# Kernel optimization log

Measured on AMD Instinct MI355X. Metric: run time of the kernel, lower is better.

The kernel has to match this reference:

```python
import jax, jax.numpy as jnp
import numpy as np

N = 4096      # num_nodes (single graph; batch is all-zeros in the original when absent)
CIN = 1024    # in_channels
H = 1024      # hidden_channels
COUT = 512    # out_channels
R = 10        # nodevec rank (hardcoded in the module)
BN_EPS = 1e-5


def setup_inputs() -> dict:
    key = jax.random.key(0)
    ks = jax.random.split(key, 8)
    w = lambda k, shp: jax.random.normal(k, shp, dtype=jnp.float32) * 0.02
    return {
        "x": jax.random.normal(ks[0], (N, CIN), dtype=jnp.float32),
        "w_map": w(ks[1], (CIN, H)),
        "b_map": jnp.zeros((H,), jnp.float32),
        "nv1": jax.random.normal(ks[2], (N, R), dtype=jnp.float32),
        "nv2": jax.random.normal(ks[3], (R, N), dtype=jnp.float32),
        "w1": w(ks[4], (H, H)),
        "b1": jnp.zeros((H,), jnp.float32),
        "w2": w(ks[5], (H, COUT)),
        "b2": jnp.zeros((COUT,), jnp.float32),
        "bn1_g": jnp.ones((H,), jnp.float32),
        "bn1_b": jnp.zeros((H,), jnp.float32),
        "bn1_m": jnp.zeros((H,), jnp.float32),
        "bn1_v": jnp.ones((H,), jnp.float32),
        "bn2_g": jnp.ones((COUT,), jnp.float32),
        "bn2_b": jnp.zeros((COUT,), jnp.float32),
        "bn2_m": jnp.zeros((COUT,), jnp.float32),
        "bn2_v": jnp.ones((COUT,), jnp.float32),
        "w_attn": w(ks[6], (COUT, 1)),
        "b_attn": jnp.zeros((1,), jnp.float32),
    }


def _batchnorm_eval(h, g, b, m, v):
    # BatchNorm1d in eval mode: running stats
    return (h - m) * jax.lax.rsqrt(v + BN_EPS) * g + b


def reference(x, w_map, b_map, nv1, nv2, w1, b1, w2, b2,
              bn1_g, bn1_b, bn1_m, bn1_v, bn2_g, bn2_b, bn2_m, bn2_v,
              w_attn, b_attn):
    # feature mapping
    xm = jax.nn.relu(x @ w_map + b_map)                       # [N, H]
    # adaptive adjacency: softmax(relu(nv1 @ nv2), dim=1) -> strictly positive,
    # so nonzero() yields the fully dense edge list; we keep it dense.
    adp = jax.nn.softmax(jax.nn.relu(nv1 @ nv2), axis=1)      # [N, N]
    # gcn_norm (PyG GCNConv default): add unit self-loops, normalize by
    # column-degree^-1/2 on both sides.
    A = adp + jnp.eye(N, dtype=adp.dtype)                      # [N, N]
    deg = jnp.sum(A, axis=0)                                   # column sums (target degree)
    dinv = jnp.where(deg > 0, jax.lax.rsqrt(deg), 0.0)
    An = (dinv[:, None] * A) * dinv[None, :]                   # D^-1/2 A D^-1/2
    # GCNConv: out_i = sum_j An[j, i] * (x W)_j + bias  =>  An^T @ (X W) + b
    h = jax.nn.relu(An.T @ (xm @ w1) + b1)                     # conv1 + relu
    h = _batchnorm_eval(h, bn1_g, bn1_b, bn1_m, bn1_v)         # bn1 (dropout off in eval)
    h = jax.nn.relu(An.T @ (h @ w2) + b2)                      # conv2 + relu
    h = _batchnorm_eval(h, bn2_g, bn2_b, bn2_m, bn2_v)         # bn2
    # global_mean_pool with batch == zeros -> single-graph mean
    pooled = jnp.mean(h, axis=0, keepdims=True)                # [1, COUT]
    attn = jax.nn.sigmoid(pooled @ w_attn + b_attn)            # [1, 1]
    return pooled * attn                                       # [1, COUT]
```

## Files before the change

kernel.cpp:

```cpp
#include <hip/hip_runtime.h>

#define NN 4096
#define R_RANK 10

typedef __bf16 bf16x8 __attribute__((ext_vector_type(8)));
typedef float floatx4 __attribute__((ext_vector_type(4)));

__device__ __forceinline__ unsigned short f2bf(float f) {
    union { float f; unsigned int u; } v; v.f = f;
    unsigned int r = v.u + 0x7FFFu + ((v.u >> 16) & 1u);
    return (unsigned short)(r >> 16);
}
__device__ __forceinline__ void gll16(const void* g, void* l) {
    __builtin_amdgcn_global_load_lds(
        (const __attribute__((address_space(1))) unsigned int*)g,
        (__attribute__((address_space(3))) unsigned int*)l, 16, 0, 0);
}
template<int N>
__device__ __forceinline__ void wait_vm() {
    if constexpr (N == 0)       asm volatile("s_waitcnt vmcnt(0)" ::: "memory");
    else if constexpr (N == 3)  asm volatile("s_waitcnt vmcnt(3)" ::: "memory");
    else if constexpr (N == 4)  asm volatile("s_waitcnt vmcnt(4)" ::: "memory");
    else if constexpr (N == 6)  asm volatile("s_waitcnt vmcnt(6)" ::: "memory");
    else if constexpr (N == 8)  asm volatile("s_waitcnt vmcnt(8)" ::: "memory");
    else static_assert(N < 0, "add vmcnt literal");
}
#define SB __builtin_amdgcn_sched_barrier(0)

__global__ __launch_bounds__(256) void row_stats_kernel(
    const float* __restrict__ nv1, const float* __restrict__ nv2,
    float* __restrict__ rowmax, float* __restrict__ rowsum,
    float* __restrict__ deg, float* __restrict__ pooled)
{
    const int i0 = blockIdx.x * 4;
    const int tid = threadIdx.x;
    if (blockIdx.x < 16) deg[blockIdx.x * 256 + tid] = 0.f;
    if (blockIdx.x >= 16 && blockIdx.x < 18) pooled[(blockIdx.x - 16) * 256 + tid] = 0.f;
    __shared__ float a[4][R_RANK];
    if (tid < 4 * R_RANK) a[tid / R_RANK][tid % R_RANK] = nv1[i0 * R_RANK + tid];
    __syncthreads();

    float s[4][16];
    float mx[4] = {0.f, 0.f, 0.f, 0.f};
    #pragma unroll
    for (int t = 0; t < 16; ++t) {
        const int j = t * 256 + tid;
        float v[R_RANK];
        #pragma unroll
        for (int r = 0; r < R_RANK; ++r) v[r] = nv2[r * NN + j];
        #pragma unroll
        for (int q = 0; q < 4; ++q) {
            float acc = 0.f;
            #pragma unroll
            for (int r = 0; r < R_RANK; ++r) acc = fmaf(a[q][r], v[r], acc);
            acc = fmaxf(acc, 0.f);
            s[q][t] = acc;
            mx[q] = fmaxf(mx[q], acc);
        }
    }
    __shared__ float red[4][4];
    #pragma unroll
    for (int q = 0; q < 4; ++q) {
        float m = mx[q];
        #pragma unroll
        for (int off = 32; off > 0; off >>= 1) m = fmaxf(m, __shfl_down(m, off, 64));
        if ((tid & 63) == 0) red[q][tid >> 6] = m;
    }
    __syncthreads();
    #pragma unroll
    for (int q = 0; q < 4; ++q)
        mx[q] = fmaxf(fmaxf(red[q][0], red[q][1]), fmaxf(red[q][2], red[q][3]));
    __syncthreads();
    float sm[4] = {0.f, 0.f, 0.f, 0.f};
    #pragma unroll
    for (int t = 0; t < 16; ++t)
        #pragma unroll
        for (int q = 0; q < 4; ++q) sm[q] += __expf(s[q][t] - mx[q]);
    #pragma unroll
    for (int q = 0; q < 4; ++q) {
        float m = sm[q];
        #pragma unroll
        for (int off = 32; off > 0; off >>= 1) m += __shfl_down(m, off, 64);
        if ((tid & 63) == 0) red[q][tid >> 6] = m;
    }
    __syncthreads();
    if (tid < 4) {
        rowmax[i0 + tid] = mx[tid];
        rowsum[i0 + tid] = red[tid][0] + red[tid][1] + red[tid][2] + red[tid][3];
    }
}

__global__ __launch_bounds__(256) void col_sum_kernel(
    const float* __restrict__ nv1, const float* __restrict__ nv2,
    const float* __restrict__ rowmax, const float* __restrict__ rowsum,
    float* __restrict__ deg)
{
    const int tid = threadIdx.x;
    const int j = blockIdx.x * 256 + tid;
    const int i0 = blockIdx.y * 64;
    __shared__ float a[64][R_RANK];
    __shared__ float rm[64], rs[64];
    if (tid < 64) {
        rm[tid] = rowmax[i0 + tid];
        rs[tid] = 1.0f / rowsum[i0 + tid];
    }
    for (int t = tid; t < 64 * R_RANK; t += 256)
        a[t / R_RANK][t % R_RANK] = nv1[i0 * R_RANK + t];
    __syncthreads();

    float v[R_RANK];
    #pragma unroll
    for (int r = 0; r < R_RANK; ++r) v[r] = nv2[r * NN + j];
    float acc = 0.f;
    #pragma unroll 4
    for (int t = 0; t < 64; ++t) {
        float s = 0.f;
        #pragma unroll
        for (int r = 0; r < R_RANK; ++r) s = fmaf(a[t][r], v[r], s);
        s = fmaxf(s, 0.f);
        acc += __expf(s - rm[t]) * rs[t];
    }
    atomicAdd(&deg[j], acc);
}

__global__ __launch_bounds__(256) void an_build_kernel(
    const float* __restrict__ nv1, const float* __restrict__ nv2,
    const float* __restrict__ rowmax, const float* __restrict__ rowsum,
    const float* __restrict__ deg, unsigned short* __restrict__ AnT)
{
    const int tid = threadIdx.x;
    const int j = blockIdx.x * 256 + tid;
    const int i0 = blockIdx.y * 8;
    __shared__ float v2s[8][R_RANK];
    __shared__ float dis[8];
    if (tid < 8 * R_RANK) {
        const int r = tid / 8, t = tid % 8;
        v2s[t][r] = nv2[r * NN + i0 + t];
    }
    if (tid < 8) dis[tid] = rsqrtf(1.0f + deg[i0 + tid]);

    float a[R_RANK];
    #pragma unroll
    for (int r = 0; r < R_RANK; ++r) a[r] = nv1[j * R_RANK + r];
    const float rm = rowmax[j];
    const float rs = 1.0f / rowsum[j];
    const float dj = rsqrtf(1.0f + deg[j]);
    __syncthreads();

    #pragma unroll
    for (int t = 0; t < 8; ++t) {
        const int i = i0 + t;
        float s = 0.f;
        #pragma unroll
        for (int r = 0; r < R_RANK; ++r) s = fmaf(a[r], v2s[t][r], s);
        s = fmaxf(s, 0.f);
        const float adp = __expf(s - rm) * rs;
        const float val = (adp + ((i == j) ? 1.f : 0.f)) * dis[t] * dj;
        AnT[(size_t)i * NN + j] = f2bf(val);
    }
}

__global__ __launch_bounds__(256) void prep_kernel(
    const float* __restrict__ x, const float* __restrict__ w_map,
    const float* __restrict__ w1, const float* __restrict__ w2,
    unsigned short* __restrict__ xb, unsigned short* __restrict__ wmT,
    unsigned short* __restrict__ w1T, unsigned short* __restrict__ w2T)
{
    const int z = blockIdx.z;
    const int tid = threadIdx.x;
    if (z == 3) {
        const int b = blockIdx.x + blockIdx.y * 32;
        const size_t base = (size_t)b * 4096 + (size_t)tid * 16;
        #pragma unroll
        for (int i = 0; i < 2; ++i) {
            const float4 a0 = *(const float4*)(x + base + i * 8);
            const float4 a1 = *(const float4*)(x + base + i * 8 + 4);
            ushort4 p, q;
            p.x = f2bf(a0.x); p.y = f2bf(a0.y); p.z = f2bf(a0.z); p.w = f2bf(a0.w);
            q.x = f2bf(a1.x); q.y = f2bf(a1.y); q.z = f2bf(a1.z); q.w = f2bf(a1.w);
            *(ushort4*)(xb + base + i * 8) = p;
            *(ushort4*)(xb + base + i * 8 + 4) = q;
        }
        return;
    }
    const float* W = (z == 0) ? w_map : (z == 1) ? w1 : w2;
    unsigned short* WT = (z == 0) ? wmT : (z == 1) ? w1T : w2T;
    const int CN = (z == 2) ? 512 : 1024;
    if (blockIdx.x * 32 >= CN) return;
    __shared__ float s[32][33];
    const int tx = tid & 31, ty = tid >> 5;
    const int r0 = blockIdx.y * 32, c0 = blockIdx.x * 32;
    #pragma unroll
    for (int i = 0; i < 4; ++i)
        s[ty + 8 * i][tx] = W[(size_t)(r0 + ty + 8 * i) * CN + c0 + tx];
    __syncthreads();
    #pragma unroll
    for (int i = 0; i < 4; ++i)
        WT[(size_t)(c0 + ty + 8 * i) * 1024 + r0 + tx] = f2bf(s[tx][ty + 8 * i]);
}

template<int OUTM, int EPI, int SK>
__global__ __launch_bounds__(512) void gemm_mfma(
    const unsigned short* __restrict__ A, const unsigned short* __restrict__ Bt,
    void* __restrict__ Out, const int M, const int N, const int K,
    const float* __restrict__ bias, const float* __restrict__ gamma,
    const float* __restrict__ beta, const float* __restrict__ mean,
    const float* __restrict__ var)
{
    __shared__ __align__(16) unsigned short As[2][8192];
    __shared__ __align__(16) unsigned short Bs[2][8192];
    const int tid = threadIdx.x;
    const int l = tid & 63, w = tid >> 6;
    const int wy = w >> 2, wx = w & 3;
    const int lr = l & 15, lq = l >> 4;

    const int gx = gridDim.x, gy = gridDim.y;
    int lin = blockIdx.x + gx * (blockIdx.y + gy * blockIdx.z);
    const int q = (gx * gy * gridDim.z) >> 3;
    lin = (lin & 7) * q + (lin >> 3);
    const int bx = lin % gx;
    const int by = (lin / gx) % gy;
    const int bz = lin / (gx * gy);

    const int row0 = by * 128, col0 = bx * 128;
    const int Kc = K / SK;
    const int kb = bz * Kc;
    const int nt = Kc >> 6;

    const unsigned short* Ag0 = A + (size_t)(row0 + w * 16 + lr) * K + kb + lq * 8;
    const unsigned short* Bg0 = Bt + (size_t)(col0 + w * 16 + lr) * K + kb + lq * 8;

    floatx4 acc[4][2];
    #pragma unroll
    for (int i = 0; i < 4; ++i)
        #pragma unroll
        for (int j = 0; j < 2; ++j) acc[i][j] = (floatx4){0.f, 0.f, 0.f, 0.f};

    #define STAGE(b, t)                                                         \
    {                                                                           \
        char* Aw = (char*)As[b] + w * 1024;                                     \
        char* Bw = (char*)Bs[b] + w * 1024;                                     \
        const int kk = (t) * 64;                                                \
        gll16(Ag0 + kk,      Aw);                                               \
        gll16(Ag0 + kk + 32, Aw + 8192);                                        \
        gll16(Bg0 + kk,      Bw);                                               \
        gll16(Bg0 + kk + 32, Bw + 8192);                                        \
    }

    STAGE(0, 0)
    for (int t = 0; t < nt; ++t) {
        if (t + 1 < nt) {
            STAGE((t + 1) & 1, t + 1)
            wait_vm<4>();
        } else {
            wait_vm<0>();
        }
        SB; __builtin_amdgcn_s_barrier(); SB;

        const char* Afr = (const char*)As[t & 1] + wy * 4096 + l * 16;
        const char* Bfr = (const char*)Bs[t & 1] + wx * 2048 + l * 16;
        #pragma unroll
        for (int h = 0; h < 2; ++h) {
            bf16x8 af[4], bf[2];
            #pragma unroll
            for (int i = 0; i < 4; ++i) af[i] = *(const bf16x8*)(Afr + h * 8192 + i * 1024);
            #pragma unroll
            for (int j = 0; j < 2; ++j) bf[j] = *(const bf16x8*)(Bfr + h * 8192 + j * 1024);
            #pragma unroll
            for (int mf = 0; mf < 4; ++mf)
                #pragma unroll
                for (int nf = 0; nf < 2; ++nf)
                    acc[mf][nf] = __builtin_amdgcn_mfma_f32_16x16x32_bf16(
                        af[mf], bf[nf], acc[mf][nf], 0, 0, 0);
        }
        SB; __builtin_amdgcn_s_barrier(); SB;
    }
    #undef STAGE

    const int gr0 = row0 + wy * 64 + lq * 4;
    const int gc0 = col0 + wx * 32 + lr;
    if constexpr (OUTM == 0) {
        float* Pz = (float*)Out + (size_t)bz * M * N;
        #pragma unroll
        for (int mf = 0; mf < 4; ++mf) {
            const int gr = gr0 + mf * 16;
            #pragma unroll
            for (int nf = 0; nf < 2; ++nf) {
                const int gc = gc0 + nf * 16;
                #pragma unroll
                for (int r = 0; r < 4; ++r)
                    Pz[(size_t)(gr + r) * N + gc] = acc[mf][nf][r];
            }
        }
    } else {
        unsigned short* O = (unsigned short*)Out;
        #pragma unroll
        for (int nf = 0; nf < 2; ++nf) {
            const int gc = gc0 + nf * 16;
            float bb = 0.f, sc = 1.f, sh = 0.f;
            if constexpr (EPI >= 1) bb = bias[gc];
            if constexpr (EPI == 2) {
                sc = gamma[gc] * rsqrtf(var[gc] + 1e-5f);
                sh = beta[gc] - mean[gc] * sc;
            }
            #pragma unroll
            for (int mf = 0; mf < 4; ++mf) {
                const int gr = gr0 + mf * 16;
                #pragma unroll
                for (int r = 0; r < 4; ++r) {
                    float xv = acc[mf][nf][r];
                    if constexpr (EPI >= 1) xv = fmaxf(xv + bb, 0.f);
                    if constexpr (EPI == 2) xv = fmaf(xv, sc, sh);
                    O[(size_t)(gr + r) * N + gc] = f2bf(xv);
                }
            }
        }
    }
}

template<int BM, int BN, int SK>
__global__ __launch_bounds__(512, 1) void gemm_big(
    const unsigned short* __restrict__ A, const unsigned short* __restrict__ Bt,
    float* __restrict__ P, const int M, const int N, const int K)
{
    constexpr int MR = BM / 32;
    constexpr int NRF = BN / 64;
    constexpr int MH = MR / 2;
    constexpr int NA = BM / 128;
    constexpr int NB = BN / 128;
    constexpr int LPT = NA + NB;
    constexpr int ABYTES = BM * 64;
    __shared__ __align__(16) unsigned short L[4][(BM + BN) * 32];
    const int tid = threadIdx.x;
    const int l = tid & 63, w = tid >> 6;
    const int wy = w >> 2, wx = w & 3;
    const int lr = l & 15, lq = l >> 4;

    const int gx = gridDim.x, gy = gridDim.y;
    int lin = blockIdx.x + gx * (blockIdx.y + gy * blockIdx.z);
    const int q = (gx * gy * gridDim.z) >> 3;
    lin = (lin & 7) * q + (lin >> 3);
    const int bx = lin % gx;
    const int by = (lin / gx) % gy;
    const int bz = lin / (gx * gy);

    const int row0 = by * BM, col0 = bx * BN;
    const int Kc = K / SK, kb = bz * Kc;
    const int nt = Kc >> 5;

    const unsigned short* Ag = A + (size_t)(row0 + w * (BM / 8) + lr) * K + kb + lq * 8;
    const unsigned short* Bg = Bt + (size_t)(col0 + w * (BN / 8) + lr) * K + kb + lq * 8;

    floatx4 acc[MR][NRF];
    #pragma unroll
    for (int i = 0; i < MR; ++i)
        #pragma unroll
        for (int j = 0; j < NRF; ++j) acc[i][j] = (floatx4){0.f, 0.f, 0.f, 0.f};

    #define STAGE_A(b, t)                                                       \
    {                                                                           \
        char* Ld = (char*)L[b];                                                 \
        const int kk = (t) * 32;                                                \
        _Pragma("unroll")                                                       \
        for (int s = 0; s < NA; ++s)                                            \
            gll16(Ag + (size_t)(s * 16) * K + kk, Ld + (w * NA + s) * 1024);    \
    }
    #define STAGE_B(b, t)                                                       \
    {                                                                           \
        char* Ld = (char*)L[b] + ABYTES;                                        \
        const int kk = (t) * 32;                                                \
        _Pragma("unroll")                                                       \
        for (int s = 0; s < NB; ++s)                                            \
            gll16(Bg + (size_t)(s * 16) * K + kk, Ld + (w * NB + s) * 1024);    \
    }

    STAGE_A(0, 0) STAGE_B(0, 0)
    STAGE_A(1, 1) STAGE_B(1, 1)
    STAGE_A(2, 2) STAGE_B(2, 2)
    for (int t = 0; t < nt; ++t) {
        if (t + 2 < nt)      wait_vm<2 * LPT>();
        else if (t + 1 < nt) wait_vm<LPT>();
        else                 wait_vm<0>();
        SB; __builtin_amdgcn_s_barrier(); SB;

        const char* Ab = (const char*)L[t & 3] + wy * (MR * 1024) + l * 16;
        const char* Bb = (const char*)L[t & 3] + ABYTES + wx * (NRF * 1024) + l * 16;

        bf16x8 bf[NRF], af0[MH];
        #pragma unroll
        for (int j = 0; j < NRF; ++j) bf[j] = *(const bf16x8*)(Bb + j * 1024);
        #pragma unroll
        for (int i = 0; i < MH; ++i) af0[i] = *(const bf16x8*)(Ab + i * 1024);
        if (t + 3 < nt) STAGE_A((t + 3) & 3, t + 3)
        __builtin_amdgcn_s_setprio(1);
        #pragma unroll
        for (int mf = 0; mf < MH; ++mf)
            #pragma unroll
            for (int nf = 0; nf < NRF; ++nf)
                acc[mf][nf] = __builtin_amdgcn_mfma_f32_16x16x32_bf16(
                    af0[mf], bf[nf], acc[mf][nf], 0, 0, 0);
        __builtin_amdgcn_s_setprio(0);
        SB; __builtin_amdgcn_s_barrier(); SB;

        bf16x8 af1[MH];
        #pragma unroll
        for (int i = 0; i < MH; ++i) af1[i] = *(const bf16x8*)(Ab + (MH + i) * 1024);
        if (t + 3 < nt) STAGE_B((t + 3) & 3, t + 3)
        __builtin_amdgcn_s_setprio(1);
        #pragma unroll
        for (int mf = 0; mf < MH; ++mf)
            #pragma unroll
            for (int nf = 0; nf < NRF; ++nf)
                acc[MH + mf][nf] = __builtin_amdgcn_mfma_f32_16x16x32_bf16(
                    af1[mf], bf[nf], acc[MH + mf][nf], 0, 0, 0);
        __builtin_amdgcn_s_setprio(0);
        SB; __builtin_amdgcn_s_barrier(); SB;
    }
    #undef STAGE_A
    #undef STAGE_B

    float* Pz = P + (size_t)bz * M * N;
    const int gr0 = row0 + wy * (BM / 2) + lq * 4;
    const int gc0 = col0 + wx * (BN / 4) + lr;
    #pragma unroll
    for (int mf = 0; mf < MR; ++mf) {
        const int gr = gr0 + mf * 16;
        #pragma unroll
        for (int nf = 0; nf < NRF; ++nf) {
            const int gc = gc0 + nf * 16;
            #pragma unroll
            for (int r = 0; r < 4; ++r)
                Pz[(size_t)(gr + r) * N + gc] = acc[mf][nf][r];
        }
    }
}

template<int EPI, int S, int NC>
__global__ __launch_bounds__(256) void reduce_k(
    const float* __restrict__ P, unsigned short* __restrict__ out, const int MN,
    const float* __restrict__ bias, const float* __restrict__ gamma,
    const float* __restrict__ beta, const float* __restrict__ mean,
    const float* __restrict__ var)
{
    const int idx = blockIdx.x * 256 + threadIdx.x;
    const int n4 = MN >> 2;
    const float4* Pv = (const float4*)P;
    float4 v = Pv[idx];
    #pragma unroll
    for (int z = 1; z < S; ++z) {
        const float4 t = Pv[idx + (size_t)z * n4];
        v.x += t.x; v.y += t.y; v.z += t.z; v.w += t.w;
    }
    float vals[4] = {v.x, v.y, v.z, v.w};
    if constexpr (EPI >= 1) {
        const int c0 = (idx << 2) & (NC - 1);
        const float4 b4 = *(const float4*)(bias + c0);
        const float bb[4] = {b4.x, b4.y, b4.z, b4.w};
        float sc[4], sh[4];
        if constexpr (EPI == 2) {
            const float4 g4 = *(const float4*)(gamma + c0);
            const float4 e4 = *(const float4*)(beta + c0);
            const float4 m4 = *(const float4*)(mean + c0);
            const float4 v4 = *(const float4*)(var + c0);
            const float gg[4] = {g4.x, g4.y, g4.z, g4.w};
            const float ee[4] = {e4.x, e4.y, e4.z, e4.w};
            const float mm[4] = {m4.x, m4.y, m4.z, m4.w};
            const float vv[4] = {v4.x, v4.y, v4.z, v4.w};
            #pragma unroll
            for (int j = 0; j < 4; ++j) {
                sc[j] = gg[j] * rsqrtf(vv[j] + 1e-5f);
                sh[j] = ee[j] - mm[j] * sc[j];
            }
        }
        #pragma unroll
        for (int j = 0; j < 4; ++j) {
            float xv = fmaxf(vals[j] + bb[j], 0.f);
            if constexpr (EPI == 2) xv = fmaf(xv, sc[j], sh[j]);
            vals[j] = xv;
        }
    }
    ushort4 p;
    p.x = f2bf(vals[0]); p.y = f2bf(vals[1]); p.z = f2bf(vals[2]); p.w = f2bf(vals[3]);
    *(ushort4*)(out + ((size_t)idx << 2)) = p;
}

template<int S>
__global__ __launch_bounds__(256) void reduce_pool_kernel(
    const float* __restrict__ P, float* __restrict__ pooled,
    const float* __restrict__ bias, const float* __restrict__ gamma,
    const float* __restrict__ beta, const float* __restrict__ mean,
    const float* __restrict__ var)
{
    const int idx = blockIdx.x * 256 + threadIdx.x;
    const int row = blockIdx.x >> 2;
    constexpr int n4 = 512 * 4096 / 4;
    const float4* Pv = (const float4*)P;
    float4 v = Pv[idx];
    #pragma unroll
    for (int z = 1; z < S; ++z) {
        const float4 t = Pv[idx + (size_t)z * n4];
        v.x += t.x; v.y += t.y; v.z += t.z; v.w += t.w;
    }
    const float b0 = bias[row];
    const float sc = gamma[row] * rsqrtf(var[row] + 1e-5f);
    const float sh = beta[row] - mean[row] * sc;
    float s = 0.f;
    const float vals[4] = {v.x, v.y, v.z, v.w};
    #pragma unroll
    for (int j = 0; j < 4; ++j)
        s += fmaf(fmaxf(vals[j] + b0, 0.f), sc, sh);
    #pragma unroll
    for (int off = 32; off > 0; off >>= 1) s += __shfl_down(s, off, 64);
    __shared__ float red[4];
    if ((threadIdx.x & 63) == 0) red[threadIdx.x >> 6] = s;
    __syncthreads();
    if (threadIdx.x == 0)
        atomicAdd(&pooled[row], red[0] + red[1] + red[2] + red[3]);
}

__global__ __launch_bounds__(512) void finalize_kernel(
    const float* __restrict__ pooled, const float* __restrict__ w_attn,
    const float* __restrict__ b_attn, float* __restrict__ out)
{
    const int c = threadIdx.x;
    __shared__ float red[512];
    const float p = pooled[c] * (1.0f / 4096.0f);
    red[c] = p * w_attn[c];
    __syncthreads();
    for (int s = 256; s > 0; s >>= 1) {
        if (c < s) red[c] += red[c + s];
        __syncthreads();
    }
    const float attn = 1.0f / (1.0f + __expf(-(red[0] + b_attn[0])));
    out[c] = p * attn;
}

extern "C" void kernel_launch(void* const* d_in, const int* in_sizes, int n_in,
                              void* d_out, int out_size, void* d_ws, size_t ws_size,
                              hipStream_t stream) {
    const float* x      = (const float*)d_in[0];
    const float* w_map  = (const float*)d_in[1];
    const float* b_map  = (const float*)d_in[2];
    const float* nv1    = (const float*)d_in[3];
    const float* nv2    = (const float*)d_in[4];
    const float* w1     = (const float*)d_in[5];
    const float* b1     = (const float*)d_in[6];
    const float* w2     = (const float*)d_in[7];
    const float* b2     = (const float*)d_in[8];
    const float* bn1_g  = (const float*)d_in[9];
    const float* bn1_b  = (const float*)d_in[10];
    const float* bn1_m  = (const float*)d_in[11];
    const float* bn1_v  = (const float*)d_in[12];
    const float* bn2_g  = (const float*)d_in[13];
    const float* bn2_b  = (const float*)d_in[14];
    const float* bn2_m  = (const float*)d_in[15];
    const float* bn2_v  = (const float*)d_in[16];
    const float* w_attn = (const float*)d_in[17];
    const float* b_attn = (const float*)d_in[18];
    float* out = (float*)d_out;

    const size_t MB = 1024 * 1024;
    const bool big = ws_size >= 118 * MB;
    char* ws = (char*)d_ws;
    unsigned short* AnT = (unsigned short*)(ws);
    float*          P   = (float*)(ws + 32 * MB);
    char* B0 = big ? (ws + 96 * MB) : (ws + 64 * MB);
    unsigned short* xb  = (unsigned short*)(B0);
    unsigned short* t1T = (unsigned short*)(B0);
    unsigned short* t2T = (unsigned short*)(B0);
    unsigned short* xm  = (unsigned short*)(B0 + 8 * MB);
    unsigned short* h1  = (unsigned short*)(B0 + 8 * MB);
    unsigned short* wmT = (unsigned short*)(B0 + 16 * MB);
    unsigned short* w1T = (unsigned short*)(B0 + 18 * MB);
    unsigned short* w2T = (unsigned short*)(B0 + 20 * MB);
    float* deg    = (float*)(B0 + 21 * MB);
    float* rowmax = deg + 4096;
    float* rowsum = rowmax + 4096;
    float* pooled = rowsum + 4096;

    prep_kernel<<<dim3(32, 32, 4), 256, 0, stream>>>(x, w_map, w1, w2, xb, wmT, w1T, w2T);
    row_stats_kernel<<<1024, 256, 0, stream>>>(nv1, nv2, rowmax, rowsum, deg, pooled);
    col_sum_kernel<<<dim3(16, 64), 256, 0, stream>>>(nv1, nv2, rowmax, rowsum, deg);
    an_build_kernel<<<dim3(16, 512), 256, 0, stream>>>(nv1, nv2, rowmax, rowsum, deg, AnT);

    gemm_mfma<1, 1, 1><<<dim3(8, 32, 1), 512, 0, stream>>>(xb, wmT, xm,
        4096, 1024, 1024, b_map, nullptr, nullptr, nullptr, nullptr);
    gemm_mfma<1, 0, 1><<<dim3(32, 8, 1), 512, 0, stream>>>(w1T, xm, t1T,
        1024, 4096, 1024, nullptr, nullptr, nullptr, nullptr, nullptr);
    if (big) {
        gemm_big<256, 256, 4><<<dim3(4, 16, 4), 512, 0, stream>>>(AnT, t1T, P, 4096, 1024, 4096);
        reduce_k<2, 4, 1024><<<4096, 256, 0, stream>>>(P, h1, 4194304,
            b1, bn1_g, bn1_b, bn1_m, bn1_v);
    } else {
        gemm_big<256, 128, 2><<<dim3(8, 16, 2), 512, 0, stream>>>(AnT, t1T, P, 4096, 1024, 4096);
        reduce_k<2, 2, 1024><<<4096, 256, 0, stream>>>(P, h1, 4194304,
            b1, bn1_g, bn1_b, bn1_m, bn1_v);
    }
    gemm_mfma<0, 0, 2><<<dim3(32, 4, 2), 512, 0, stream>>>(w2T, h1, P,
        512, 4096, 1024, nullptr, nullptr, nullptr, nullptr, nullptr);
    reduce_k<0, 2, 1><<<2048, 256, 0, stream>>>(P, t2T, 2097152,
        nullptr, nullptr, nullptr, nullptr, nullptr);
    if (big) {
        gemm_big<256, 256, 8><<<dim3(16, 2, 8), 512, 0, stream>>>(t2T, AnT, P, 512, 4096, 4096);
        reduce_pool_kernel<8><<<2048, 256, 0, stream>>>(
            P, pooled, b2, bn2_g, bn2_b, bn2_m, bn2_v);
    } else {
        gemm_big<128, 256, 4><<<dim3(16, 4, 4), 512, 0, stream>>>(t2T, AnT, P, 512, 4096, 4096);
        reduce_pool_kernel<4><<<2048, 256, 0, stream>>>(
            P, pooled, b2, bn2_g, bn2_b, bn2_m, bn2_v);
    }

    finalize_kernel<<<1, 512, 0, stream>>>(pooled, w_attn, b_attn, out);
}
```

Measured before the change: 312.0 us.

## Restructure big GEMM to 3-stage pipeline with one barrier and smaller tiles

The big split-K GEMM drops from a 4-buffer to a 3-buffer LDS ring with rotating indices. It now issues the combined A+B prefetch for tile t+2 at the top of each iteration and removes the mid-iteration barrier. Launch bounds rise to allow up to 4 blocks per CU, and the An-multiply launches switch to 256x128 tiles with more blocks. The aim is more occupancy and less synchronisation per K-step, at the cost of a shallower prefetch and less reuse per tile.

```diff
diff --git a/kernel.cpp b/kernel.cpp
--- a/kernel.cpp
+++ b/kernel.cpp
@@ -319,7 +319,7 @@
 }
 
 template<int BM, int BN, int SK>
-__global__ __launch_bounds__(512, 1) void gemm_big(
+__global__ __launch_bounds__(512, 4) void gemm_big(
     const unsigned short* __restrict__ A, const unsigned short* __restrict__ Bt,
     float* __restrict__ P, const int M, const int N, const int K)
 {
@@ -330,7 +330,7 @@
     constexpr int NB = BN / 128;
     constexpr int LPT = NA + NB;
     constexpr int ABYTES = BM * 64;
-    __shared__ __align__(16) unsigned short L[4][(BM + BN) * 32];
+    __shared__ __align__(16) unsigned short L[3][(BM + BN) * 32];
     const int tid = threadIdx.x;
     const int l = tid & 63, w = tid >> 6;
     const int wy = w >> 2, wx = w & 3;
@@ -357,41 +357,41 @@
         #pragma unroll
         for (int j = 0; j < NRF; ++j) acc[i][j] = (floatx4){0.f, 0.f, 0.f, 0.f};
 
-    #define STAGE_A(b, t)                                                       \
+    #define STAGEB(b, t)                                                        \
     {                                                                           \
         char* Ld = (char*)L[b];                                                 \
         const int kk = (t) * 32;                                                \
         _Pragma("unroll")                                                       \
         for (int s = 0; s < NA; ++s)                                            \
             gll16(Ag + (size_t)(s * 16) * K + kk, Ld + (w * NA + s) * 1024);    \
-    }
-    #define STAGE_B(b, t)                                                       \
-    {                                                                           \
-        char* Ld = (char*)L[b] + ABYTES;                                        \
-        const int kk = (t) * 32;                                                \
         _Pragma("unroll")                                                       \
         for (int s = 0; s < NB; ++s)                                            \
-            gll16(Bg + (size_t)(s * 16) * K + kk, Ld + (w * NB + s) * 1024);    \
-    }
-
-    STAGE_A(0, 0) STAGE_B(0, 0)
-    STAGE_A(1, 1) STAGE_B(1, 1)
-    STAGE_A(2, 2) STAGE_B(2, 2)
+            gll16(Bg + (size_t)(s * 16) * K + kk,                               \
+                  Ld + ABYTES + (w * NB + s) * 1024);                           \
+    }
+
+    STAGEB(0, 0)
+    STAGEB(1, 1)
+    int b0 = 0, b1 = 1, b2 = 2;
     for (int t = 0; t < nt; ++t) {
-        if (t + 2 < nt)      wait_vm<2 * LPT>();
-        else if (t + 1 < nt) wait_vm<LPT>();
-        else                 wait_vm<0>();
+        if (t + 2 < nt) {
+            STAGEB(b2, t + 2)
+            wait_vm<2 * LPT>();
+        } else if (t + 1 < nt) {
+            wait_vm<LPT>();
+        } else {
+            wait_vm<0>();
+        }
         SB; __builtin_amdgcn_s_barrier(); SB;
 
-        const char* Ab = (const char*)L[t & 3] + wy * (MR * 1024) + l * 16;
-        const char* Bb = (const char*)L[t & 3] + ABYTES + wx * (NRF * 1024) + l * 16;
+        const char* Ab = (const char*)L[b0] + wy * (MR * 1024) + l * 16;
+        const char* Bb = (const char*)L[b0] + ABYTES + wx * (NRF * 1024) + l * 16;
 
         bf16x8 bf[NRF], af0[MH];
         #pragma unroll
         for (int j = 0; j < NRF; ++j) bf[j] = *(const bf16x8*)(Bb + j * 1024);
         #pragma unroll
         for (int i = 0; i < MH; ++i) af0[i] = *(const bf16x8*)(Ab + i * 1024);
-        if (t + 3 < nt) STAGE_A((t + 3) & 3, t + 3)
         __builtin_amdgcn_s_setprio(1);
         #pragma unroll
         for (int mf = 0; mf < MH; ++mf)
@@ -400,12 +400,9 @@
                 acc[mf][nf] = __builtin_amdgcn_mfma_f32_16x16x32_bf16(
                     af0[mf], bf[nf], acc[mf][nf], 0, 0, 0);
         __builtin_amdgcn_s_setprio(0);
-        SB; __builtin_amdgcn_s_barrier(); SB;
-
         bf16x8 af1[MH];
         #pragma unroll
         for (int i = 0; i < MH; ++i) af1[i] = *(const bf16x8*)(Ab + (MH + i) * 1024);
-        if (t + 3 < nt) STAGE_B((t + 3) & 3, t + 3)
         __builtin_amdgcn_s_setprio(1);
         #pragma unroll
         for (int mf = 0; mf < MH; ++mf)
@@ -415,9 +412,9 @@
                     af1[mf], bf[nf], acc[MH + mf][nf], 0, 0, 0);
         __builtin_amdgcn_s_setprio(0);
         SB; __builtin_amdgcn_s_barrier(); SB;
-    }
-    #undef STAGE_A
-    #undef STAGE_B
+        const int tmp = b0; b0 = b1; b1 = b2; b2 = tmp;
+    }
+    #undef STAGEB
 
     float* Pz = P + (size_t)bz * M * N;
     const int gr0 = row0 + wy * (BM / 2) + lq * 4;
@@ -588,7 +585,7 @@
     gemm_mfma<1, 0, 1><<<dim3(32, 8, 1), 512, 0, stream>>>(w1T, xm, t1T,
         1024, 4096, 1024, nullptr, nullptr, nullptr, nullptr, nullptr);
     if (big) {
-        gemm_big<256, 256, 4><<<dim3(4, 16, 4), 512, 0, stream>>>(AnT, t1T, P, 4096, 1024, 4096);
+        gemm_big<256, 128, 4><<<dim3(8, 16, 4), 512, 0, stream>>>(AnT, t1T, P, 4096, 1024, 4096);
         reduce_k<2, 4, 1024><<<4096, 256, 0, stream>>>(P, h1, 4194304,
             b1, bn1_g, bn1_b, bn1_m, bn1_v);
     } else {
@@ -601,11 +598,11 @@
     reduce_k<0, 2, 1><<<2048, 256, 0, stream>>>(P, t2T, 2097152,
         nullptr, nullptr, nullptr, nullptr, nullptr);
     if (big) {
-        gemm_big<256, 256, 8><<<dim3(16, 2, 8), 512, 0, stream>>>(t2T, AnT, P, 512, 4096, 4096);
+        gemm_big<256, 128, 8><<<dim3(32, 2, 8), 512, 0, stream>>>(t2T, AnT, P, 512, 4096, 4096);
         reduce_pool_kernel<8><<<2048, 256, 0, stream>>>(
             P, pooled, b2, bn2_g, bn2_b, bn2_m, bn2_v);
     } else {
-        gemm_big<128, 256, 4><<<dim3(16, 4, 4), 512, 0, stream>>>(t2T, AnT, P, 512, 4096, 4096);
+        gemm_big<256, 128, 4><<<dim3(32, 2, 4), 512, 0, stream>>>(t2T, AnT, P, 512, 4096, 4096);
         reduce_pool_kernel<4><<<2048, 256, 0, stream>>>(
             P, pooled, b2, bn2_g, bn2_b, bn2_m, bn2_v);
     }
```

After: 325.1 us. 1.04x slower.
